# Optimization experiments

Measured on AMD Instinct MI355X. Metric: run time of the kernel, lower is better.

## Reference

```python
import jax, jax.numpy as jnp
import numpy as np

N_NODES = 100000
N_EDGES = 1600000
IN_DIM, HID_DIM, LAT_DIM = 256, 128, 64


def setup_inputs() -> dict:
    key = jax.random.key(0)
    ks = jax.random.split(key, 10)
    x = jax.random.normal(ks[0], (N_NODES, IN_DIM), dtype=jnp.float32)
    edge_index = jax.random.randint(ks[1], (2, N_EDGES), 0, N_NODES, dtype=jnp.int32)
    s = 1.0 / np.sqrt(IN_DIM)
    W1 = jax.random.normal(ks[2], (IN_DIM, HID_DIM), dtype=jnp.float32) * s
    b1 = jnp.zeros((HID_DIM,), dtype=jnp.float32)
    s2 = 1.0 / np.sqrt(HID_DIM)
    Wmu = jax.random.normal(ks[3], (HID_DIM, LAT_DIM), dtype=jnp.float32) * s2
    bmu = jnp.zeros((LAT_DIM,), dtype=jnp.float32)
    Wls = jax.random.normal(ks[4], (HID_DIM, LAT_DIM), dtype=jnp.float32) * s2
    bls = jnp.zeros((LAT_DIM,), dtype=jnp.float32)
    eps = jax.random.normal(ks[5], (N_NODES, LAT_DIM), dtype=jnp.float32)
    return {"x": x, "edge_index": edge_index, "W1": W1, "b1": b1,
            "Wmu": Wmu, "bmu": bmu, "Wls": Wls, "bls": bls, "eps": eps}


def _gcn_norm(edge_index, n_nodes):
    # PyG GCNConv: add self-loops, symmetric normalization D^-1/2 A D^-1/2
    loops = jnp.arange(n_nodes, dtype=edge_index.dtype)
    src = jnp.concatenate([edge_index[0], loops])
    dst = jnp.concatenate([edge_index[1], loops])
    ones = jnp.ones(src.shape[0], dtype=jnp.float32)
    deg = jax.ops.segment_sum(ones, dst, num_segments=n_nodes)
    dinv = jnp.where(deg > 0, jax.lax.rsqrt(deg), 0.0)
    norm = dinv[src] * dinv[dst]  # [E + N]
    return src, dst, norm


def _gcn_conv(x, src, dst, norm, W, b, n_nodes):
    h = x @ W                       # transform first (in_dim >= out_dim)
    msg = h[src] * norm[:, None]    # gather + scale per edge
    out = jax.ops.segment_sum(msg, dst, num_segments=n_nodes)  # scatter-add
    return out + b


def reference(x, edge_index, W1, b1, Wmu, bmu, Wls, bls, eps):
    n = x.shape[0]
    src, dst, norm = _gcn_norm(edge_index, n)
    hidden = jax.nn.relu(_gcn_conv(x, src, dst, norm, W1, b1, n))
    mu = _gcn_conv(hidden, src, dst, norm, Wmu, bmu, n)
    logstd = _gcn_conv(hidden, src, dst, norm, Wls, bls, n)
    # reparameterize (training mode): z = mu + eps * exp(logstd)
    z = mu + eps * jnp.exp(logstd)
    return (z, mu, logstd)
```

## Files before the change

kernel.cpp:

```cpp
#include <hip/hip_runtime.h>
#include <cstdint>
#include <cstddef>

typedef __attribute__((ext_vector_type(8))) short short8v;
typedef __attribute__((ext_vector_type(4))) float f32x4;

#define BSHIFT 9
#define NBUCK_MAX 256
#define BCAP 16384
#define F8SCALE 16.0f
#define F8INV   0.0625f

__device__ __forceinline__ unsigned short f2bf_rne(float x) {
    unsigned int u = __float_as_uint(x);
    return (unsigned short)((u + 0x7fffu + ((u >> 16) & 1u)) >> 16);
}

__device__ __forceinline__ short8v pack_bf16x8(float4 a, float4 b) {
    unsigned int u0, u1, u2, u3;
    asm("v_cvt_pk_bf16_f32 %0, %1, %2" : "=v"(u0) : "v"(a.x), "v"(a.y));
    asm("v_cvt_pk_bf16_f32 %0, %1, %2" : "=v"(u1) : "v"(a.z), "v"(a.w));
    asm("v_cvt_pk_bf16_f32 %0, %1, %2" : "=v"(u2) : "v"(b.x), "v"(b.y));
    asm("v_cvt_pk_bf16_f32 %0, %1, %2" : "=v"(u3) : "v"(b.z), "v"(b.w));
    uint4 r = make_uint4(u0, u1, u2, u3);
    return *(short8v*)&r;
}

__device__ __forceinline__ unsigned int pk_fp8(float a, float b, float c, float d) {
    int r = 0;
    r = __builtin_amdgcn_cvt_pk_fp8_f32(a, b, r, false);
    r = __builtin_amdgcn_cvt_pk_fp8_f32(c, d, r, true);
    return (unsigned int)r;
}
__device__ __forceinline__ void accf8(float* a, uint2 v) {
    auto p0 = __builtin_amdgcn_cvt_pk_f32_fp8((int)v.x, false);
    auto p1 = __builtin_amdgcn_cvt_pk_f32_fp8((int)v.x, true);
    auto p2 = __builtin_amdgcn_cvt_pk_f32_fp8((int)v.y, false);
    auto p3 = __builtin_amdgcn_cvt_pk_f32_fp8((int)v.y, true);
    a[0] += p0[0]; a[1] += p0[1];
    a[2] += p1[0]; a[3] += p1[1];
    a[4] += p2[0]; a[5] += p2[1];
    a[6] += p3[0]; a[7] += p3[1];
}


__global__ __launch_bounds__(256) void k_prepB(const float* __restrict__ W1,
                                               const float* __restrict__ Wmu,
                                               const float* __restrict__ Wls,
                                               unsigned short* __restrict__ B1h,
                                               unsigned short* __restrict__ B2t,
                                               int* __restrict__ bcur) {
    int i = blockIdx.x * 256 + threadIdx.x;
    if (blockIdx.x == 0 && threadIdx.x < NBUCK_MAX) bcur[threadIdx.x] = 0;
    if (i < 256 * 128) {
        int k = i >> 7, c = i & 127;
        int ch = ((c & 15) << 3) | (c >> 4);
        B1h[c * 256 + k] = f2bf_rne(W1[k * 128 + ch]);
    }
    if (i < 128 * 128) {
        int k = i >> 7, och = i & 127;
        float vv = (och < 64) ? Wmu[k * 64 + och] : Wls[k * 64 + (och - 64)];
        B2t[och * 128 + k] = f2bf_rne(vv);
    }
}


__global__ __launch_bounds__(256) void k_scatb(const int* __restrict__ srcv,
                                               const int* __restrict__ dstv,
                                               int* __restrict__ bcur,
                                               unsigned int* __restrict__ ebuf, int E) {
    __shared__ int hcnt[NBUCK_MAX], hbase[NBUCK_MAX], hcur[NBUCK_MAX];
    int t = threadIdx.x;
    for (int b = t; b < NBUCK_MAX; b += 256) { hcnt[b] = 0; hcur[b] = 0; }
    __syncthreads();
    int base = blockIdx.x * 4096;
    for (int q = 0; q < 16; ++q) {
        int i = base + q * 256 + t;
        if (i < E) atomicAdd(&hcnt[dstv[i] >> BSHIFT], 1);
    }
    __syncthreads();
    for (int b = t; b < NBUCK_MAX; b += 256)
        hbase[b] = hcnt[b] ? atomicAdd(&bcur[b], hcnt[b]) : 0;
    __syncthreads();
    for (int q = 0; q < 16; ++q) {
        int i = base + q * 256 + t;
        if (i < E) {
            int d = dstv[i], b = d >> BSHIFT;
            int off = hbase[b] + atomicAdd(&hcur[b], 1);
            if (off < BCAP)
                ebuf[(size_t)b * BCAP + off] = ((unsigned)srcv[i] << 9) | (unsigned)(d & 511);
        }
    }
}

__global__ __launch_bounds__(512) void k_bsort(const unsigned int* __restrict__ ebuf,
                                               const int* __restrict__ bcur,
                                               int* __restrict__ colv,
                                               int* __restrict__ rowstart,
                                               int* __restrict__ rowend,
                                               float* __restrict__ dinv, int n) {
    __shared__ int cnt[512], sc[512], cur[512];
    int t = threadIdx.x;
    int b = blockIdx.x;
    int node0 = b << BSHIFT;
    int nn = min(512, n - node0);
    int s0 = (int)((size_t)b * BCAP);
    int total = min(bcur[b], BCAP);
    cnt[t] = 0;
    __syncthreads();
    for (int i = t; i < total; i += 512)
        atomicAdd(&cnt[ebuf[s0 + i] & 511u], 1);
    __syncthreads();
    int v = cnt[t];
    sc[t] = v;
    __syncthreads();
    for (int off = 1; off < 512; off <<= 1) {
        int x = 0;
        if (t >= off) x = sc[t - off];
        __syncthreads();
        if (t >= off) sc[t] += x;
        __syncthreads();
    }
    if (t < nn) {
        int rs = s0 + sc[t] - v;
        cur[t] = rs;
        rowstart[node0 + t] = rs;
        rowend[node0 + t] = rs + v;
        dinv[node0 + t] = rsqrtf((float)(v + 1));
    }
    __syncthreads();
    for (int i = t; i < total; i += 512) {
        unsigned int pv = ebuf[s0 + i];
        int pos = atomicAdd(&cur[pv & 511u], 1);
        colv[pos] = (int)(pv >> 9);
    }
}


__global__ __launch_bounds__(256) void k_gemm1(const float* __restrict__ A,
                                               const unsigned short* __restrict__ Bth,
                                               const float* __restrict__ dinv,
                                               unsigned char* __restrict__ Cf8, int M) {
    const int K = 256;
    __shared__ unsigned short Bs[128 * 128];
    const int tid = threadIdx.x;
    const int w = tid >> 6, l = tid & 63;
    const int lr = l & 15, lq = l >> 4;
    const int row0 = blockIdx.x * 64 + w * 16;

    int rg = row0 + lr;
    const float* ap = A + (size_t)(rg < M ? rg : 0) * K + lq * 8;

    float4 ar[8][2];
#pragma unroll
    for (int s = 0; s < 8; ++s) {
        ar[s][0] = *(const float4*)(ap + s * 32);
        ar[s][1] = *(const float4*)(ap + s * 32 + 4);
    }

    f32x4 acc[8];
#pragma unroll
    for (int ct = 0; ct < 8; ++ct) acc[ct] = (f32x4){0.f, 0.f, 0.f, 0.f};

#pragma unroll
    for (int h = 0; h < 2; ++h) {
        if (h) __syncthreads();
#pragma unroll
        for (int r = 0; r < 8; ++r) {
            int rw = r * 4 + w;
            int sl = rw >> 3, ct = rw & 7;
            short8v v = *(const short8v*)(Bth + (size_t)(ct * 16 + lr) * K + (h * 4 + sl) * 32 + lq * 8);
            *(short8v*)(&Bs[(rw * 64 + l) * 8]) = v;
        }
        __syncthreads();

#pragma unroll
        for (int sl = 0; sl < 4; ++sl) {
            int sg = h * 4 + sl;
            short8v ah = pack_bf16x8(ar[sg][0], ar[sg][1]);
#pragma unroll
            for (int ct = 0; ct < 8; ++ct) {
                short8v bh = *(const short8v*)(&Bs[((sl * 8 + ct) * 64 + l) * 8]);
                acc[ct] = __builtin_amdgcn_mfma_f32_16x16x32_bf16(ah, bh, acc[ct], 0, 0, 0);
            }
        }
    }

    int rbase = row0 + (lq << 2);
#pragma unroll
    for (int j = 0; j < 4; ++j) {
        int row = rbase + j;
        if (row < M) {
            float dv = dinv[row] * F8SCALE;
            uint2 r;
            r.x = pk_fp8(dv * acc[0][j], dv * acc[1][j], dv * acc[2][j], dv * acc[3][j]);
            r.y = pk_fp8(dv * acc[4][j], dv * acc[5][j], dv * acc[6][j], dv * acc[7][j]);
            *(uint2*)(Cf8 + (size_t)row * 128 + lr * 8) = r;
        }
    }
}


__global__ __launch_bounds__(256) void k_prop1(const unsigned char* __restrict__ hf,
                                               const int* __restrict__ colv,
                                               const int* __restrict__ rowstart,
                                               const int* __restrict__ rowend,
                                               const float* __restrict__ dinv,
                                               const float* __restrict__ bias,
                                               unsigned char* __restrict__ of, int n) {
    int wid = (blockIdx.x * 256 + threadIdx.x) >> 6;
    int nid = wid * 4 + ((threadIdx.x >> 4) & 3);
    if (nid >= n) return;
    int cl = threadIdx.x & 15;
    const unsigned char* hp = hf + cl * 8;
    int s = rowstart[nid], e = rowend[nid];
    float a[8] = {0.f, 0.f, 0.f, 0.f, 0.f, 0.f, 0.f, 0.f};
    int i = s;
    for (; i + 4 <= e; i += 4) {
        int c0 = colv[i], c1 = colv[i + 1], c2 = colv[i + 2], c3 = colv[i + 3];
        uint2 v0 = *(const uint2*)(hp + (size_t)c0 * 128);
        uint2 v1 = *(const uint2*)(hp + (size_t)c1 * 128);
        uint2 v2 = *(const uint2*)(hp + (size_t)c2 * 128);
        uint2 v3 = *(const uint2*)(hp + (size_t)c3 * 128);
        accf8(a, v0); accf8(a, v1); accf8(a, v2); accf8(a, v3);
    }
    for (; i < e; ++i) {
        int c = colv[i];
        uint2 v = *(const uint2*)(hp + (size_t)c * 128);
        accf8(a, v);
    }
    uint2 vo = *(const uint2*)(hp + (size_t)nid * 128);
    accf8(a, vo);
    float dv = dinv[nid];
    float din = dv * F8INV;
    float dos = dv * F8SCALE;
    float4 b0 = *(const float4*)(bias + cl * 8);
    float4 b1v = *(const float4*)(bias + cl * 8 + 4);
    float bb[8] = {b0.x, b0.y, b0.z, b0.w, b1v.x, b1v.y, b1v.z, b1v.w};
    float o[8];
#pragma unroll
    for (int k = 0; k < 8; ++k)
        o[k] = fmaxf(a[k] * din + bb[k], 0.f) * dos;
    uint2 r;
    r.x = pk_fp8(o[0], o[1], o[2], o[3]);
    r.y = pk_fp8(o[4], o[5], o[6], o[7]);
    *(uint2*)(of + (size_t)nid * 128 + cl * 8) = r;
}


__global__ __launch_bounds__(256) void k_prop2z(const unsigned char* __restrict__ hf,
                                                const int* __restrict__ colv,
                                                const int* __restrict__ rowstart,
                                                const int* __restrict__ rowend,
                                                const float* __restrict__ dinv,
                                                const unsigned short* __restrict__ B2t,
                                                const float* __restrict__ bmu,
                                                const float* __restrict__ bls,
                                                const float* __restrict__ eps,
                                                float* __restrict__ zout,
                                                float* __restrict__ muout,
                                                float* __restrict__ lsout, int n) {
    __shared__ unsigned short aggb[4][16][136];
    const int tid = threadIdx.x;
    const int w = tid >> 6, l = tid & 63;
    const int wbase = blockIdx.x * 64 + w * 16;

    const int g = (l >> 4) & 3, cl = l & 15;
    const unsigned char* hp = hf + cl * 8;
    for (int p = 0; p < 4; ++p) {
        int slot = p * 4 + g;
        int nid = wbase + slot;
        float a[8] = {0.f, 0.f, 0.f, 0.f, 0.f, 0.f, 0.f, 0.f};
        float dv = 0.f;
        if (nid < n) {
            int s = rowstart[nid], e = rowend[nid];
            int i = s;
            for (; i + 4 <= e; i += 4) {
                int c0 = colv[i], c1 = colv[i + 1], c2 = colv[i + 2], c3 = colv[i + 3];
                uint2 v0 = *(const uint2*)(hp + (size_t)c0 * 128);
                uint2 v1 = *(const uint2*)(hp + (size_t)c1 * 128);
                uint2 v2 = *(const uint2*)(hp + (size_t)c2 * 128);
                uint2 v3 = *(const uint2*)(hp + (size_t)c3 * 128);
                accf8(a, v0); accf8(a, v1); accf8(a, v2); accf8(a, v3);
            }
            for (; i < e; ++i) {
                int c = colv[i];
                uint2 v = *(const uint2*)(hp + (size_t)c * 128);
                accf8(a, v);
            }
            uint2 vo = *(const uint2*)(hp + (size_t)nid * 128);
            accf8(a, vo);
            dv = dinv[nid] * F8INV;
        }
        short8v r;
#pragma unroll
        for (int k = 0; k < 8; ++k) r[k] = (short)f2bf_rne(a[k] * dv);
        *(short8v*)(&aggb[w][slot][cl * 8]) = r;
    }
    asm volatile("s_waitcnt lgkmcnt(0)" ::: "memory");
    __builtin_amdgcn_sched_barrier(0);

    const int lr = l & 15, lq = l >> 4;
    f32x4 accD[8];
#pragma unroll
    for (int t = 0; t < 8; ++t) accD[t] = (f32x4){0.f, 0.f, 0.f, 0.f};
#pragma unroll
    for (int sl = 0; sl < 4; ++sl) {
        short8v af = *(const short8v*)(&aggb[w][lr][sl * 32 + lq * 8]);
#pragma unroll
        for (int t = 0; t < 8; ++t) {
            short8v bt = *(const short8v*)(B2t + (size_t)(t * 16 + lr) * 128 + sl * 32 + lq * 8);
            accD[t] = __builtin_amdgcn_mfma_f32_16x16x32_bf16(af, bt, accD[t], 0, 0, 0);
        }
    }

#pragma unroll
    for (int t = 0; t < 4; ++t) {
        int och = t * 16 + lr;
        float bmv = bmu[och], blv = bls[och];
#pragma unroll
        for (int j = 0; j < 4; ++j) {
            int nid = wbase + lq * 4 + j;
            if (nid < n) {
                float mu = accD[t][j] + bmv;
                float ls = accD[t + 4][j] + blv;
                size_t o = (size_t)nid * 64 + och;
                float z = mu + eps[o] * __expf(ls);
                zout[o] = z;
                muout[o] = mu;
                lsout[o] = ls;
            }
        }
    }
}


extern "C" void kernel_launch(void* const* d_in, const int* in_sizes, int n_in,
                              void* d_out, int out_size, void* d_ws, size_t ws_size,
                              hipStream_t stream) {
    const float* x   = (const float*)d_in[0];
    const int*   ei  = (const int*)d_in[1];
    const float* W1  = (const float*)d_in[2];
    const float* b1  = (const float*)d_in[3];
    const float* Wmu = (const float*)d_in[4];
    const float* bmu = (const float*)d_in[5];
    const float* Wls = (const float*)d_in[6];
    const float* bls = (const float*)d_in[7];
    const float* eps = (const float*)d_in[8];

    const int n = in_sizes[0] / 256;
    const int E = in_sizes[1] / 2;
    const int* srcv = ei;
    const int* dstv = ei + E;
    const int nbuck = (n + 511) >> BSHIFT;

    char* w = (char*)d_ws;
    auto alloc = [&](size_t bytes) -> char* {
        char* p = w;
        w += (bytes + 255) & ~(size_t)255;
        return p;
    };
    float* dinv     = (float*)alloc((size_t)n * 4);
    int*   rowstart = (int*)alloc((size_t)n * 4);
    int*   rowend   = (int*)alloc((size_t)n * 4);
    int*   bcur     = (int*)alloc((size_t)NBUCK_MAX * 4);
    unsigned int* ebuf = (unsigned int*)alloc((size_t)nbuck * BCAP * 4);
    int*   colv     = (int*)alloc((size_t)nbuck * BCAP * 4);
    unsigned short* B1h = (unsigned short*)alloc(128 * 256 * 2);
    unsigned short* B2t = (unsigned short*)alloc(128 * 128 * 2);
    unsigned char* hf8   = (unsigned char*)alloc((size_t)n * 128);
    unsigned char* hidf8 = (unsigned char*)alloc((size_t)n * 128);

    const int ecb = (E + 4095) / 4096;

    k_prepB<<<128, 256, 0, stream>>>(W1, Wmu, Wls, B1h, B2t, bcur);
    k_scatb<<<ecb, 256, 0, stream>>>(srcv, dstv, bcur, ebuf, E);
    k_bsort<<<nbuck, 512, 0, stream>>>(ebuf, bcur, colv, rowstart, rowend, dinv, n);

    k_gemm1<<<(n + 63) / 64, 256, 0, stream>>>(x, B1h, dinv, hf8, n);
    k_prop1<<<(n + 15) / 16, 256, 0, stream>>>(hf8, colv, rowstart, rowend, dinv, b1, hidf8, n);

    float* zout  = (float*)d_out;
    float* muout = zout + (size_t)n * 64;
    float* lsout = muout + (size_t)n * 64;
    k_prop2z<<<(n + 63) / 64, 256, 0, stream>>>(hidf8, colv, rowstart, rowend, dinv,
                                                B2t, bmu, bls, eps,
                                                zout, muout, lsout, n);
}
```

Before: 211.9 us.

## Feed gathered aggregates straight into MFMA registers and skip LDS staging in prop2z

The layer-2 kernel used to gather neighbor rows with 16 lanes per node, stage the bf16 aggregates in shared memory, and reload them as MFMA operands. Now each lane owns one node and one 8-channel group per 32-channel slice, so the gathered sums already sit in MFMA B-operand layout. The weights become the A operand, which transposes the output so each lane writes float4 runs of mu, logstd and z. This removes the LDS round trip and makes the epilogue stores vectorized. In exchange each lane issues four strided 8-byte loads per edge, and work per lane now follows a single node's degree, which can increase divergence across the wave.

```diff
diff --git a/kernel.cpp b/kernel.cpp
--- a/kernel.cpp
+++ b/kernel.cpp
@@ -260,76 +260,91 @@
                                                 float* __restrict__ zout,
                                                 float* __restrict__ muout,
                                                 float* __restrict__ lsout, int n) {
-    __shared__ unsigned short aggb[4][16][136];
     const int tid = threadIdx.x;
-    const int w = tid >> 6, l = tid & 63;
-    const int wbase = blockIdx.x * 64 + w * 16;
-
-    const int g = (l >> 4) & 3, cl = l & 15;
-    const unsigned char* hp = hf + cl * 8;
-    for (int p = 0; p < 4; ++p) {
-        int slot = p * 4 + g;
-        int nid = wbase + slot;
-        float a[8] = {0.f, 0.f, 0.f, 0.f, 0.f, 0.f, 0.f, 0.f};
-        float dv = 0.f;
-        if (nid < n) {
-            int s = rowstart[nid], e = rowend[nid];
-            int i = s;
-            for (; i + 4 <= e; i += 4) {
-                int c0 = colv[i], c1 = colv[i + 1], c2 = colv[i + 2], c3 = colv[i + 3];
-                uint2 v0 = *(const uint2*)(hp + (size_t)c0 * 128);
-                uint2 v1 = *(const uint2*)(hp + (size_t)c1 * 128);
-                uint2 v2 = *(const uint2*)(hp + (size_t)c2 * 128);
-                uint2 v3 = *(const uint2*)(hp + (size_t)c3 * 128);
-                accf8(a, v0); accf8(a, v1); accf8(a, v2); accf8(a, v3);
-            }
-            for (; i < e; ++i) {
-                int c = colv[i];
-                uint2 v = *(const uint2*)(hp + (size_t)c * 128);
-                accf8(a, v);
-            }
-            uint2 vo = *(const uint2*)(hp + (size_t)nid * 128);
-            accf8(a, vo);
-            dv = dinv[nid] * F8INV;
-        }
-        short8v r;
-#pragma unroll
-        for (int k = 0; k < 8; ++k) r[k] = (short)f2bf_rne(a[k] * dv);
-        *(short8v*)(&aggb[w][slot][cl * 8]) = r;
-    }
-    asm volatile("s_waitcnt lgkmcnt(0)" ::: "memory");
-    __builtin_amdgcn_sched_barrier(0);
-
-    const int lr = l & 15, lq = l >> 4;
+    const int l = tid & 63;
+    const int nl = l & 15;
+    const int kc = l >> 4;
+    int wid = (blockIdx.x * 256 + tid) >> 6;
+    int nid = wid * 16 + nl;
+    bool valid = nid < n;
+    int nidc = valid ? nid : 0;
+
+    int s = valid ? rowstart[nid] : 0;
+    int e = valid ? rowend[nid] : 0;
+
+    float a[4][8] = {{0.f}};
+    const unsigned char* hp = hf + kc * 8;
+    int i = s;
+    for (; i + 2 <= e; i += 2) {
+        int c0 = colv[i], c1 = colv[i + 1];
+        uint2 v00 = *(const uint2*)(hp + (size_t)c0 * 128);
+        uint2 v01 = *(const uint2*)(hp + (size_t)c0 * 128 + 32);
+        uint2 v02 = *(const uint2*)(hp + (size_t)c0 * 128 + 64);
+        uint2 v03 = *(const uint2*)(hp + (size_t)c0 * 128 + 96);
+        uint2 v10 = *(const uint2*)(hp + (size_t)c1 * 128);
+        uint2 v11 = *(const uint2*)(hp + (size_t)c1 * 128 + 32);
+        uint2 v12 = *(const uint2*)(hp + (size_t)c1 * 128 + 64);
+        uint2 v13 = *(const uint2*)(hp + (size_t)c1 * 128 + 96);
+        accf8(a[0], v00); accf8(a[1], v01); accf8(a[2], v02); accf8(a[3], v03);
+        accf8(a[0], v10); accf8(a[1], v11); accf8(a[2], v12); accf8(a[3], v13);
+    }
+    if (i < e) {
+        int c = colv[i];
+        uint2 v0 = *(const uint2*)(hp + (size_t)c * 128);
+        uint2 v1 = *(const uint2*)(hp + (size_t)c * 128 + 32);
+        uint2 v2 = *(const uint2*)(hp + (size_t)c * 128 + 64);
+        uint2 v3 = *(const uint2*)(hp + (size_t)c * 128 + 96);
+        accf8(a[0], v0); accf8(a[1], v1); accf8(a[2], v2); accf8(a[3], v3);
+    }
+    {
+        uint2 v0 = *(const uint2*)(hp + (size_t)nidc * 128);
+        uint2 v1 = *(const uint2*)(hp + (size_t)nidc * 128 + 32);
+        uint2 v2 = *(const uint2*)(hp + (size_t)nidc * 128 + 64);
+        uint2 v3 = *(const uint2*)(hp + (size_t)nidc * 128 + 96);
+        accf8(a[0], v0); accf8(a[1], v1); accf8(a[2], v2); accf8(a[3], v3);
+    }
+    float dv = valid ? dinv[nid] * F8INV : 0.f;
+
+    short8v bAgg[4];
+#pragma unroll
+    for (int s4 = 0; s4 < 4; ++s4)
+#pragma unroll
+        for (int q = 0; q < 8; ++q)
+            bAgg[s4][q] = (short)f2bf_rne(a[s4][q] * dv);
+
     f32x4 accD[8];
 #pragma unroll
     for (int t = 0; t < 8; ++t) accD[t] = (f32x4){0.f, 0.f, 0.f, 0.f};
-#pragma unroll
-    for (int sl = 0; sl < 4; ++sl) {
-        short8v af = *(const short8v*)(&aggb[w][lr][sl * 32 + lq * 8]);
+
+#pragma unroll
+    for (int s4 = 0; s4 < 4; ++s4) {
 #pragma unroll
         for (int t = 0; t < 8; ++t) {
-            short8v bt = *(const short8v*)(B2t + (size_t)(t * 16 + lr) * 128 + sl * 32 + lq * 8);
-            accD[t] = __builtin_amdgcn_mfma_f32_16x16x32_bf16(af, bt, accD[t], 0, 0, 0);
-        }
-    }
-
-#pragma unroll
-    for (int t = 0; t < 4; ++t) {
-        int och = t * 16 + lr;
-        float bmv = bmu[och], blv = bls[och];
-#pragma unroll
-        for (int j = 0; j < 4; ++j) {
-            int nid = wbase + lq * 4 + j;
-            if (nid < n) {
-                float mu = accD[t][j] + bmv;
-                float ls = accD[t + 4][j] + blv;
-                size_t o = (size_t)nid * 64 + och;
-                float z = mu + eps[o] * __expf(ls);
-                zout[o] = z;
-                muout[o] = mu;
-                lsout[o] = ls;
-            }
+            short8v aW = *(const short8v*)(B2t + (size_t)(t * 16 + nl) * 128 + s4 * 32 + kc * 8);
+            accD[t] = __builtin_amdgcn_mfma_f32_16x16x32_bf16(aW, bAgg[s4], accD[t], 0, 0, 0);
+        }
+    }
+
+    if (valid) {
+#pragma unroll
+        for (int t = 0; t < 4; ++t) {
+            int och0 = t * 16 + kc * 4;
+            float4 bm4 = *(const float4*)(bmu + och0);
+            float4 bl4 = *(const float4*)(bls + och0);
+            float4 mu4, ls4, z4;
+            mu4.x = accD[t][0] + bm4.x; mu4.y = accD[t][1] + bm4.y;
+            mu4.z = accD[t][2] + bm4.z; mu4.w = accD[t][3] + bm4.w;
+            ls4.x = accD[t + 4][0] + bl4.x; ls4.y = accD[t + 4][1] + bl4.y;
+            ls4.z = accD[t + 4][2] + bl4.z; ls4.w = accD[t + 4][3] + bl4.w;
+            size_t o = (size_t)nid * 64 + och0;
+            float4 e4 = *(const float4*)(eps + o);
+            z4.x = mu4.x + e4.x * __expf(ls4.x);
+            z4.y = mu4.y + e4.y * __expf(ls4.y);
+            z4.z = mu4.z + e4.z * __expf(ls4.z);
+            z4.w = mu4.w + e4.w * __expf(ls4.w);
+            *(float4*)(zout + o)  = z4;
+            *(float4*)(muout + o) = mu4;
+            *(float4*)(lsout + o) = ls4;
         }
     }
 }
```

Result: slower. 223.9 us (+5.7%).
